# Kernel optimization log

Measured on AMD Instinct MI355X. Metric: run time of the kernel, lower is better.

## Reference

```python
import jax, jax.numpy as jnp
import numpy as np

N_NODES = 100000

def _sage_conv(x, src, dst, W_l, b_l, W_r):
    # PyG SAGEConv(aggr='mean'): out = lin_l(mean_{j in N(i)} x_j) + lin_r(x_i)
    agg = jax.ops.segment_sum(x[src], dst, num_segments=N_NODES)          # [N, F]
    cnt = jax.ops.segment_sum(jnp.ones_like(dst, dtype=x.dtype), dst,
                              num_segments=N_NODES)                        # [N]
    mean = agg / jnp.maximum(cnt, 1.0)[:, None]
    return mean @ W_l + b_l + x @ W_r

def setup_inputs() -> dict:
    key = jax.random.key(0)
    ks = jax.random.split(key, 10)
    F_in, H = 128, 16
    E, P = 1600000, 2000000
    x = jax.random.normal(ks[0], (N_NODES, F_in), dtype=jnp.float32)
    edge_index = jax.random.randint(ks[1], (2, E), 0, N_NODES, dtype=jnp.int64)
    decode_index = jax.random.randint(ks[2], (2, P), 0, N_NODES, dtype=jnp.int64)
    s1 = 1.0 / np.sqrt(F_in)
    s2 = 1.0 / np.sqrt(H)
    W1l = jax.random.uniform(ks[3], (F_in, H), jnp.float32, -s1, s1)
    b1 = jax.random.uniform(ks[4], (H,), jnp.float32, -s1, s1)
    W1r = jax.random.uniform(ks[5], (F_in, H), jnp.float32, -s1, s1)
    W2l = jax.random.uniform(ks[6], (H, H), jnp.float32, -s2, s2)
    b2 = jax.random.uniform(ks[7], (H,), jnp.float32, -s2, s2)
    W2r = jax.random.uniform(ks[8], (H, H), jnp.float32, -s2, s2)
    return {"x": x, "W1l": W1l, "b1": b1, "W1r": W1r,
            "W2l": W2l, "b2": b2, "W2r": W2r,
            "edge_index": edge_index, "decode_index": decode_index}

def reference(x, W1l, b1, W1r, W2l, b2, W2r, edge_index, decode_index):
    src, dst = edge_index[0], edge_index[1]
    h = _sage_conv(x, src, dst, W1l, b1, W1r)          # conv1
    h = jax.nn.relu(h)                                  # relu (dropout: eval -> identity)
    h = _sage_conv(h, src, dst, W2l, b2, W2r)           # conv2
    logits = jnp.sum(h[decode_index[0]] * h[decode_index[1]], axis=1)  # [P]
    return jax.nn.sigmoid(logits)
```

## Files before the change

kernel.cpp:

```cpp
#include <hip/hip_runtime.h>
#include <hip/hip_fp16.h>

#define N_NODES 100000
#define F_IN 128
#define H 16
#define NBIN 391
#define BINCAP 4608
#define ECHUNK 2048
#define LIN1B 782
#define QSCALE 4096.0f
#define QINV (1.0f / 4096.0f)

__device__ inline unsigned int packi16(float a, float b) {
  int ia = __float2int_rn(fminf(fmaxf(a * QSCALE, -32767.f), 32767.f));
  int ib = __float2int_rn(fminf(fmaxf(b * QSCALE, -32767.f), 32767.f));
  return (unsigned int)((ia & 0xffff) | (ib << 16));
}

__global__ void __launch_bounds__(512) k_init(int* __restrict__ binCur) {
  int t = threadIdx.x;
  if (t < NBIN) binCur[t] = t * BINCAP;
}

__global__ void __launch_bounds__(256) k_front(
    const float* __restrict__ x, const float* __restrict__ W1l,
    const float* __restrict__ W1r, unsigned short* __restrict__ y1l,
    float* __restrict__ y1r, const int* __restrict__ src,
    const int* __restrict__ dst, int* __restrict__ binCur,
    int* __restrict__ recs, int E) {
  __shared__ float smem[2 * H * 128];
  int t = threadIdx.x;
  if (blockIdx.x < LIN1B) {
    float* red = smem;
    int part = __builtin_amdgcn_readfirstlane(t >> 7);
    int ln = t & 127;
    int n = blockIdx.x * 128 + ln;
    int nc = (n < N_NODES) ? n : (N_NODES - 1);
    const float4* xr = (const float4*)(x + (size_t)nc * F_IN + part * (F_IN / 2));
    float4 xv[16];
#pragma unroll
    for (int j = 0; j < 16; ++j) xv[j] = xr[j];
    const float* Wl = W1l + part * (F_IN / 2) * H;
    const float* Wr = W1r + part * (F_IN / 2) * H;
    float al[H], ar[H];
#pragma unroll
    for (int c = 0; c < H; ++c) { al[c] = 0.f; ar[c] = 0.f; }
#pragma unroll
    for (int j = 0; j < 16; ++j) {
      float xs[4] = {xv[j].x, xv[j].y, xv[j].z, xv[j].w};
#pragma unroll
      for (int jj = 0; jj < 4; ++jj) {
        int k = j * 4 + jj;
#pragma unroll
        for (int c = 0; c < H; ++c) {
          al[c] = fmaf(xs[jj], Wl[k * H + c], al[c]);
          ar[c] = fmaf(xs[jj], Wr[k * H + c], ar[c]);
        }
      }
    }
    if (part == 1) {
#pragma unroll
      for (int c = 0; c < H; ++c) {
        red[c * 128 + ln] = al[c];
        red[(H + c) * 128 + ln] = ar[c];
      }
    }
    __syncthreads();
    if (part == 0 && n < N_NODES) {
#pragma unroll
      for (int c = 0; c < H; ++c) {
        al[c] += red[c * 128 + ln];
        ar[c] += red[(H + c) * 128 + ln];
      }
      uint4 w0, w1;
      w0.x = packi16(al[0], al[1]);  w0.y = packi16(al[2], al[3]);
      w0.z = packi16(al[4], al[5]);  w0.w = packi16(al[6], al[7]);
      w1.x = packi16(al[8], al[9]);  w1.y = packi16(al[10], al[11]);
      w1.z = packi16(al[12], al[13]); w1.w = packi16(al[14], al[15]);
      uint4* ol = (uint4*)(y1l + (size_t)n * H);
      ol[0] = w0;
      ol[1] = w1;
      float4* orr = (float4*)(y1r + (size_t)n * H);
#pragma unroll
      for (int q = 0; q < 4; ++q)
        orr[q] = make_float4(ar[4 * q], ar[4 * q + 1], ar[4 * q + 2], ar[4 * q + 3]);
    }
  } else {
    int* hist = (int*)smem;
    int* gbase = hist + 512;
    int* cnt2 = gbase + 512;
    hist[t] = 0; hist[256 + t] = 0;
    cnt2[t] = 0; cnt2[256 + t] = 0;
    __syncthreads();
    int base = (blockIdx.x - LIN1B) * ECHUNK;
    int rec[8], bin[8];
#pragma unroll
    for (int j = 0; j < 8; ++j) {
      int e = base + j * 256 + t;
      if (e < E) {
        int s = src[e];
        int d = dst[e];
        rec[j] = (s << 8) | (d & 255);
        bin[j] = d >> 8;
        atomicAdd(&hist[bin[j]], 1);
      } else {
        bin[j] = -1;
      }
    }
    __syncthreads();
    for (int u = t; u < NBIN; u += 256) {
      int c = hist[u];
      gbase[u] = (c > 0) ? atomicAdd(&binCur[u], c) : 0;
    }
    __syncthreads();
#pragma unroll
    for (int j = 0; j < 8; ++j) {
      if (bin[j] >= 0) {
        int loc = atomicAdd(&cnt2[bin[j]], 1);
        int slot = gbase[bin[j]] + loc;
        if (slot < (bin[j] + 1) * BINCAP)
          recs[slot] = rec[j];
      }
    }
  }
}

__global__ void __launch_bounds__(512) k_group(
    int* __restrict__ recs, const int* __restrict__ binCur,
    int* __restrict__ deg, int* __restrict__ rowBeg) {
  __shared__ int lrec[BINCAP];
  __shared__ int hist[256];
  __shared__ int off[256];
  __shared__ int cur[256];
  int t = threadIdx.x;
  int b = blockIdx.x;
  int rbase = b * BINCAP;
  int R = binCur[b] - rbase;
  if (R > BINCAP) R = BINCAP;
  if (t < 256) hist[t] = 0;
  __syncthreads();
#pragma unroll
  for (int j = 0; j < 9; ++j) {
    int idx = j * 512 + t;
    if (idx < R) {
      int r = recs[rbase + idx];
      lrec[idx] = r;
      atomicAdd(&hist[r & 255], 1);
    }
  }
  __syncthreads();
  if (t < 256) off[t] = hist[t];
  __syncthreads();
  for (int o = 1; o < 256; o <<= 1) {
    int u = 0;
    if (t < 256 && t >= o) u = off[t - o];
    __syncthreads();
    if (t < 256) off[t] += u;
    __syncthreads();
  }
  if (t < 256) {
    int ex = off[t] - hist[t];
    cur[t] = ex;
    int n = (b << 8) + t;
    if (n < N_NODES) {
      deg[n] = hist[t];
      rowBeg[n] = rbase + ex;
    }
  }
  __syncthreads();
#pragma unroll
  for (int j = 0; j < 9; ++j) {
    int idx = j * 512 + t;
    if (idx < R) {
      int r = lrec[idx];
      int slot = atomicAdd(&cur[r & 255], 1);
      recs[rbase + slot] = r >> 8;
    }
  }
}

__global__ void __launch_bounds__(256) k_gather1(
    const int* __restrict__ srcSorted, const int* __restrict__ deg,
    const int* __restrict__ rowBeg, const unsigned short* __restrict__ y1l,
    const float* __restrict__ y1r, const float* __restrict__ b1,
    const float* __restrict__ W2l, const float* __restrict__ W2r,
    unsigned short* __restrict__ z2l, float* __restrict__ z2r) {
  int tid = blockIdx.x * 256 + threadIdx.x;
  int n = tid >> 2;
  int q = tid & 3;
  if (n >= N_NODES) return;
  int beg = rowBeg[n];
  int dg = deg[n];
  int end = beg + dg;
  int acc0 = 0, acc1 = 0, acc2 = 0, acc3 = 0;
  int i = beg;
  for (; i + 8 <= end; i += 8) {
    int sqa = srcSorted[i + q];
    int sqb = srcSorted[i + 4 + q];
#pragma unroll
    for (int j = 0; j < 4; ++j) {
      int sa = __shfl(sqa, j, 4);
      int sb = __shfl(sqb, j, 4);
      uint2 va = *(const uint2*)(y1l + (size_t)sa * H + q * 4);
      uint2 vb = *(const uint2*)(y1l + (size_t)sb * H + q * 4);
      acc0 += (((int)(va.x << 16)) >> 16) + (((int)(vb.x << 16)) >> 16);
      acc1 += (((int)va.x) >> 16) + (((int)vb.x) >> 16);
      acc2 += (((int)(va.y << 16)) >> 16) + (((int)(vb.y << 16)) >> 16);
      acc3 += (((int)va.y) >> 16) + (((int)vb.y) >> 16);
    }
  }
  for (; i + 4 <= end; i += 4) {
    int sq = srcSorted[i + q];
#pragma unroll
    for (int j = 0; j < 4; ++j) {
      int sj = __shfl(sq, j, 4);
      uint2 v = *(const uint2*)(y1l + (size_t)sj * H + q * 4);
      acc0 += ((int)(v.x << 16)) >> 16;
      acc1 += ((int)v.x) >> 16;
      acc2 += ((int)(v.y << 16)) >> 16;
      acc3 += ((int)v.y) >> 16;
    }
  }
  for (; i < end; ++i) {
    int sj = srcSorted[i];
    uint2 v = *(const uint2*)(y1l + (size_t)sj * H + q * 4);
    acc0 += ((int)(v.x << 16)) >> 16;
    acc1 += ((int)v.x) >> 16;
    acc2 += ((int)(v.y << 16)) >> 16;
    acc3 += ((int)v.y) >> 16;
  }
  float s = (1.f / fmaxf((float)dg, 1.f)) * QINV;
  float4 yr = *(const float4*)(y1r + (size_t)n * H + q * 4);
  float4 bb = *(const float4*)(b1 + q * 4);
  float h1x = fmaxf(fmaf((float)acc0, s, bb.x + yr.x), 0.f);
  float h1y = fmaxf(fmaf((float)acc1, s, bb.y + yr.y), 0.f);
  float h1z = fmaxf(fmaf((float)acc2, s, bb.z + yr.z), 0.f);
  float h1w = fmaxf(fmaf((float)acc3, s, bb.w + yr.w), 0.f);
  float zl0 = 0.f, zl1 = 0.f, zl2 = 0.f, zl3 = 0.f;
  float zr0 = 0.f, zr1 = 0.f, zr2 = 0.f, zr3 = 0.f;
#pragma unroll
  for (int sl = 0; sl < 4; ++sl) {
    float hx = __shfl(h1x, sl, 4);
    float hy = __shfl(h1y, sl, 4);
    float hz = __shfl(h1z, sl, 4);
    float hw = __shfl(h1w, sl, 4);
    float hk4[4] = {hx, hy, hz, hw};
#pragma unroll
    for (int j = 0; j < 4; ++j) {
      int k = sl * 4 + j;
      float4 wl = *(const float4*)(W2l + k * H + q * 4);
      float4 wr = *(const float4*)(W2r + k * H + q * 4);
      float hk = hk4[j];
      zl0 = fmaf(hk, wl.x, zl0); zl1 = fmaf(hk, wl.y, zl1);
      zl2 = fmaf(hk, wl.z, zl2); zl3 = fmaf(hk, wl.w, zl3);
      zr0 = fmaf(hk, wr.x, zr0); zr1 = fmaf(hk, wr.y, zr1);
      zr2 = fmaf(hk, wr.z, zr2); zr3 = fmaf(hk, wr.w, zr3);
    }
  }
  uint2 pk;
  pk.x = packi16(zl0, zl1);
  pk.y = packi16(zl2, zl3);
  *(uint2*)(z2l + (size_t)n * H + q * 4) = pk;
  *(float4*)(z2r + (size_t)n * H + q * 4) = make_float4(zr0, zr1, zr2, zr3);
}

__global__ void __launch_bounds__(256) k_gather2(
    const int* __restrict__ srcSorted, const int* __restrict__ deg,
    const int* __restrict__ rowBeg, const unsigned short* __restrict__ z2l,
    const float* __restrict__ z2r, const float* __restrict__ b2,
    __half* __restrict__ h2) {
  int tid = blockIdx.x * 256 + threadIdx.x;
  int n = tid >> 2;
  int q = tid & 3;
  if (n >= N_NODES) return;
  int beg = rowBeg[n];
  int dg = deg[n];
  int end = beg + dg;
  int acc0 = 0, acc1 = 0, acc2 = 0, acc3 = 0;
  int i = beg;
  for (; i + 8 <= end; i += 8) {
    int sqa = srcSorted[i + q];
    int sqb = srcSorted[i + 4 + q];
#pragma unroll
    for (int j = 0; j < 4; ++j) {
      int sa = __shfl(sqa, j, 4);
      int sb = __shfl(sqb, j, 4);
      uint2 va = *(const uint2*)(z2l + (size_t)sa * H + q * 4);
      uint2 vb = *(const uint2*)(z2l + (size_t)sb * H + q * 4);
      acc0 += (((int)(va.x << 16)) >> 16) + (((int)(vb.x << 16)) >> 16);
      acc1 += (((int)va.x) >> 16) + (((int)vb.x) >> 16);
      acc2 += (((int)(va.y << 16)) >> 16) + (((int)(vb.y << 16)) >> 16);
      acc3 += (((int)va.y) >> 16) + (((int)vb.y) >> 16);
    }
  }
  for (; i + 4 <= end; i += 4) {
    int sq = srcSorted[i + q];
#pragma unroll
    for (int j = 0; j < 4; ++j) {
      int sj = __shfl(sq, j, 4);
      uint2 v = *(const uint2*)(z2l + (size_t)sj * H + q * 4);
      acc0 += ((int)(v.x << 16)) >> 16;
      acc1 += ((int)v.x) >> 16;
      acc2 += ((int)(v.y << 16)) >> 16;
      acc3 += ((int)v.y) >> 16;
    }
  }
  for (; i < end; ++i) {
    int sj = srcSorted[i];
    uint2 v = *(const uint2*)(z2l + (size_t)sj * H + q * 4);
    acc0 += ((int)(v.x << 16)) >> 16;
    acc1 += ((int)v.x) >> 16;
    acc2 += ((int)(v.y << 16)) >> 16;
    acc3 += ((int)v.y) >> 16;
  }
  float s = (1.f / fmaxf((float)dg, 1.f)) * QINV;
  float4 zr = *(const float4*)(z2r + (size_t)n * H + q * 4);
  float4 bb = *(const float4*)(b2 + q * 4);
  float v0 = fmaf((float)acc0, s, bb.x + zr.x);
  float v1 = fmaf((float)acc1, s, bb.y + zr.y);
  float v2 = fmaf((float)acc2, s, bb.z + zr.z);
  float v3 = fmaf((float)acc3, s, bb.w + zr.w);
  __half2 h0 = __floats2half2_rn(v0, v1);
  __half2 h1 = __floats2half2_rn(v2, v3);
  uint2 pk;
  pk.x = *(unsigned int*)&h0;
  pk.y = *(unsigned int*)&h1;
  *(uint2*)(h2 + (size_t)n * H + q * 4) = pk;
}

__device__ inline float dot8h(uint4 u, uint4 v) {
  float acc = 0.f;
  const unsigned int* uw = (const unsigned int*)&u;
  const unsigned int* vw = (const unsigned int*)&v;
#pragma unroll
  for (int j = 0; j < 4; ++j) {
    float2 a = __half22float2(*(const __half2*)&uw[j]);
    float2 b = __half22float2(*(const __half2*)&vw[j]);
    acc = fmaf(a.x, b.x, acc);
    acc = fmaf(a.y, b.y, acc);
  }
  return acc;
}

__global__ void __launch_bounds__(256) k_decode(
    const int* __restrict__ ps, const int* __restrict__ pd,
    const __half* __restrict__ h2, float* __restrict__ out, int P) {
  int t = blockIdx.x * 256 + threadIdx.x;
  int p = t * 2;
  if (p >= P) return;
  int2 av = *(const int2*)(ps + p);
  int2 bv = *(const int2*)(pd + p);
  const uint4* ha0 = (const uint4*)(h2 + (size_t)av.x * H);
  const uint4* hb0 = (const uint4*)(h2 + (size_t)bv.x * H);
  const uint4* ha1 = (const uint4*)(h2 + (size_t)av.y * H);
  const uint4* hb1 = (const uint4*)(h2 + (size_t)bv.y * H);
  uint4 u00 = ha0[0], u01 = ha0[1];
  uint4 v00 = hb0[0], v01 = hb0[1];
  uint4 u10 = ha1[0], u11 = ha1[1];
  uint4 v10 = hb1[0], v11 = hb1[1];
  float d0 = dot8h(u00, v00) + dot8h(u01, v01);
  float d1 = dot8h(u10, v10) + dot8h(u11, v11);
  float o0 = 1.f / (1.f + __expf(-d0));
  float o1 = 1.f / (1.f + __expf(-d1));
  if (p + 1 < P) {
    *(float2*)(out + p) = make_float2(o0, o1);
  } else {
    out[p] = o0;
  }
}

extern "C" void kernel_launch(void* const* d_in, const int* in_sizes, int n_in,
                              void* d_out, int out_size, void* d_ws, size_t ws_size,
                              hipStream_t stream) {
  const float* x   = (const float*)d_in[0];
  const float* W1l = (const float*)d_in[1];
  const float* b1  = (const float*)d_in[2];
  const float* W1r = (const float*)d_in[3];
  const float* W2l = (const float*)d_in[4];
  const float* b2  = (const float*)d_in[5];
  const float* W2r = (const float*)d_in[6];
  const int* ei = (const int*)d_in[7];
  const int* di = (const int*)d_in[8];
  const int E = in_sizes[7] / 2;
  const int P = in_sizes[8] / 2;

  const size_t NF = (size_t)N_NODES * H;
  unsigned short* y1l = (unsigned short*)d_ws;
  __half*         h2  = (__half*)y1l;
  unsigned short* z2l = y1l + NF;
  float*  y1r = (float*)(z2l + NF);
  float*  z2r = y1r;
  int* recs   = (int*)(y1r + NF);
  int* binCur = recs + (size_t)NBIN * BINCAP;
  int* deg    = binCur + 512;
  int* rowBeg = deg + N_NODES;

  const int fillBlocks = (E + ECHUNK - 1) / ECHUNK;
  const int frontBlocks = LIN1B + fillBlocks;
  const int gatherBlocks = ((N_NODES * 4) + 255) / 256;
  const int decodeBlocks = ((P + 1) / 2 + 255) / 256;

  k_init<<<1, 512, 0, stream>>>(binCur);
  k_front<<<frontBlocks, 256, 0, stream>>>(x, W1l, W1r, y1l, y1r,
                                           ei, ei + E, binCur, recs, E);
  k_group<<<NBIN, 512, 0, stream>>>(recs, binCur, deg, rowBeg);
  k_gather1<<<gatherBlocks, 256, 0, stream>>>(recs, deg, rowBeg, y1l, y1r,
                                              b1, W2l, W2r, z2l, z2r);
  k_gather2<<<gatherBlocks, 256, 0, stream>>>(recs, deg, rowBeg, z2l, z2r,
                                              b2, h2);
  k_decode<<<decodeBlocks, 256, 0, stream>>>(di, di + P, h2, (float*)d_out, P);
}
```

Measured before the change: 225.5 us.

## Split fused front kernel into separate lin1 and edge bin-fill kernels

Splits the combined kernel, which ran the dense first-layer projection and the edge binning in one launch, into two launches. The projection now handles 64 nodes per block with the 128 input features split four ways across threads instead of two, and combines the partial sums through shared memory. The binning kernel now processes 8192 edges per 512-thread block, which cuts the number of global atomics on the bin cursors. The split gives up the overlap between the compute-bound and atomic-bound work that the fused launch allowed, and adds one extra launch.

After: 213.6 us. 1.06x faster.

```diff
diff --git a/kernel.cpp b/kernel.cpp
--- a/kernel.cpp
+++ b/kernel.cpp
@@ -6,8 +6,7 @@
 #define H 16
 #define NBIN 391
 #define BINCAP 4608
-#define ECHUNK 2048
-#define LIN1B 782
+#define ECHUNK 8192
 #define QSCALE 4096.0f
 #define QINV (1.0f / 4096.0f)
 
@@ -22,105 +21,108 @@
   if (t < NBIN) binCur[t] = t * BINCAP;
 }
 
-__global__ void __launch_bounds__(256) k_front(
+__global__ void __launch_bounds__(256) k_lin1(
     const float* __restrict__ x, const float* __restrict__ W1l,
     const float* __restrict__ W1r, unsigned short* __restrict__ y1l,
-    float* __restrict__ y1r, const int* __restrict__ src,
-    const int* __restrict__ dst, int* __restrict__ binCur,
-    int* __restrict__ recs, int E) {
-  __shared__ float smem[2 * H * 128];
+    float* __restrict__ y1r) {
+  __shared__ float red[3 * 32 * 64];
   int t = threadIdx.x;
-  if (blockIdx.x < LIN1B) {
-    float* red = smem;
-    int part = __builtin_amdgcn_readfirstlane(t >> 7);
-    int ln = t & 127;
-    int n = blockIdx.x * 128 + ln;
-    int nc = (n < N_NODES) ? n : (N_NODES - 1);
-    const float4* xr = (const float4*)(x + (size_t)nc * F_IN + part * (F_IN / 2));
-    float4 xv[16];
-#pragma unroll
-    for (int j = 0; j < 16; ++j) xv[j] = xr[j];
-    const float* Wl = W1l + part * (F_IN / 2) * H;
-    const float* Wr = W1r + part * (F_IN / 2) * H;
-    float al[H], ar[H];
-#pragma unroll
-    for (int c = 0; c < H; ++c) { al[c] = 0.f; ar[c] = 0.f; }
-#pragma unroll
-    for (int j = 0; j < 16; ++j) {
-      float xs[4] = {xv[j].x, xv[j].y, xv[j].z, xv[j].w};
-#pragma unroll
-      for (int jj = 0; jj < 4; ++jj) {
-        int k = j * 4 + jj;
-#pragma unroll
-        for (int c = 0; c < H; ++c) {
-          al[c] = fmaf(xs[jj], Wl[k * H + c], al[c]);
-          ar[c] = fmaf(xs[jj], Wr[k * H + c], ar[c]);
-        }
+  int part = __builtin_amdgcn_readfirstlane(t >> 6);
+  int ln = t & 63;
+  int n = blockIdx.x * 64 + ln;
+  int nc = (n < N_NODES) ? n : (N_NODES - 1);
+  const float4* xr = (const float4*)(x + (size_t)nc * F_IN + part * (F_IN / 4));
+  float4 xv[8];
+#pragma unroll
+  for (int j = 0; j < 8; ++j) xv[j] = xr[j];
+  const float* Wl = W1l + part * (F_IN / 4) * H;
+  const float* Wr = W1r + part * (F_IN / 4) * H;
+  float al[H], ar[H];
+#pragma unroll
+  for (int c = 0; c < H; ++c) { al[c] = 0.f; ar[c] = 0.f; }
+#pragma unroll
+  for (int j = 0; j < 8; ++j) {
+    float xs[4] = {xv[j].x, xv[j].y, xv[j].z, xv[j].w};
+#pragma unroll
+    for (int jj = 0; jj < 4; ++jj) {
+      int k = j * 4 + jj;
+#pragma unroll
+      for (int c = 0; c < H; ++c) {
+        al[c] = fmaf(xs[jj], Wl[k * H + c], al[c]);
+        ar[c] = fmaf(xs[jj], Wr[k * H + c], ar[c]);
       }
     }
-    if (part == 1) {
-#pragma unroll
-      for (int c = 0; c < H; ++c) {
-        red[c * 128 + ln] = al[c];
-        red[(H + c) * 128 + ln] = ar[c];
-      }
-    }
-    __syncthreads();
-    if (part == 0 && n < N_NODES) {
-#pragma unroll
-      for (int c = 0; c < H; ++c) {
-        al[c] += red[c * 128 + ln];
-        ar[c] += red[(H + c) * 128 + ln];
-      }
-      uint4 w0, w1;
-      w0.x = packi16(al[0], al[1]);  w0.y = packi16(al[2], al[3]);
-      w0.z = packi16(al[4], al[5]);  w0.w = packi16(al[6], al[7]);
-      w1.x = packi16(al[8], al[9]);  w1.y = packi16(al[10], al[11]);
-      w1.z = packi16(al[12], al[13]); w1.w = packi16(al[14], al[15]);
-      uint4* ol = (uint4*)(y1l + (size_t)n * H);
-      ol[0] = w0;
-      ol[1] = w1;
-      float4* orr = (float4*)(y1r + (size_t)n * H);
-#pragma unroll
-      for (int q = 0; q < 4; ++q)
-        orr[q] = make_float4(ar[4 * q], ar[4 * q + 1], ar[4 * q + 2], ar[4 * q + 3]);
-    }
-  } else {
-    int* hist = (int*)smem;
-    int* gbase = hist + 512;
-    int* cnt2 = gbase + 512;
-    hist[t] = 0; hist[256 + t] = 0;
-    cnt2[t] = 0; cnt2[256 + t] = 0;
-    __syncthreads();
-    int base = (blockIdx.x - LIN1B) * ECHUNK;
-    int rec[8], bin[8];
-#pragma unroll
-    for (int j = 0; j < 8; ++j) {
-      int e = base + j * 256 + t;
-      if (e < E) {
-        int s = src[e];
-        int d = dst[e];
-        rec[j] = (s << 8) | (d & 255);
-        bin[j] = d >> 8;
-        atomicAdd(&hist[bin[j]], 1);
-      } else {
-        bin[j] = -1;
-      }
-    }
-    __syncthreads();
-    for (int u = t; u < NBIN; u += 256) {
-      int c = hist[u];
-      gbase[u] = (c > 0) ? atomicAdd(&binCur[u], c) : 0;
-    }
-    __syncthreads();
-#pragma unroll
-    for (int j = 0; j < 8; ++j) {
-      if (bin[j] >= 0) {
-        int loc = atomicAdd(&cnt2[bin[j]], 1);
-        int slot = gbase[bin[j]] + loc;
-        if (slot < (bin[j] + 1) * BINCAP)
-          recs[slot] = rec[j];
-      }
+  }
+  if (part != 0) {
+    int base = (part - 1) * 2048;
+#pragma unroll
+    for (int c = 0; c < H; ++c) {
+      red[base + c * 64 + ln] = al[c];
+      red[base + (H + c) * 64 + ln] = ar[c];
+    }
+  }
+  __syncthreads();
+  if (part == 0 && n < N_NODES) {
+#pragma unroll
+    for (int c = 0; c < H; ++c) {
+      al[c] = ((al[c] + red[c * 64 + ln]) + red[2048 + c * 64 + ln])
+              + red[4096 + c * 64 + ln];
+      ar[c] = ((ar[c] + red[(H + c) * 64 + ln]) + red[2048 + (H + c) * 64 + ln])
+              + red[4096 + (H + c) * 64 + ln];
+    }
+    uint4 w0, w1;
+    w0.x = packi16(al[0], al[1]);  w0.y = packi16(al[2], al[3]);
+    w0.z = packi16(al[4], al[5]);  w0.w = packi16(al[6], al[7]);
+    w1.x = packi16(al[8], al[9]);  w1.y = packi16(al[10], al[11]);
+    w1.z = packi16(al[12], al[13]); w1.w = packi16(al[14], al[15]);
+    uint4* ol = (uint4*)(y1l + (size_t)n * H);
+    ol[0] = w0;
+    ol[1] = w1;
+    float4* orr = (float4*)(y1r + (size_t)n * H);
+#pragma unroll
+    for (int q = 0; q < 4; ++q)
+      orr[q] = make_float4(ar[4 * q], ar[4 * q + 1], ar[4 * q + 2], ar[4 * q + 3]);
+  }
+}
+
+__global__ void __launch_bounds__(512) k_binfill(
+    const int* __restrict__ src, const int* __restrict__ dst,
+    int* __restrict__ binCur, int* __restrict__ recs, int E) {
+  __shared__ int hist[512];
+  __shared__ int gbase[512];
+  __shared__ int cnt2[512];
+  int t = threadIdx.x;
+  hist[t] = 0;
+  cnt2[t] = 0;
+  __syncthreads();
+  int base = blockIdx.x * ECHUNK;
+  int rec[16], bin[16];
+#pragma unroll
+  for (int j = 0; j < 16; ++j) {
+    int e = base + j * 512 + t;
+    if (e < E) {
+      int s = src[e];
+      int d = dst[e];
+      rec[j] = (s << 8) | (d & 255);
+      bin[j] = d >> 8;
+      atomicAdd(&hist[bin[j]], 1);
+    } else {
+      bin[j] = -1;
+    }
+  }
+  __syncthreads();
+  if (t < NBIN) {
+    int c = hist[t];
+    gbase[t] = (c > 0) ? atomicAdd(&binCur[t], c) : 0;
+  }
+  __syncthreads();
+#pragma unroll
+  for (int j = 0; j < 16; ++j) {
+    if (bin[j] >= 0) {
+      int loc = atomicAdd(&cnt2[bin[j]], 1);
+      int slot = gbase[bin[j]] + loc;
+      if (slot < (bin[j] + 1) * BINCAP)
+        recs[slot] = rec[j];
     }
   }
 }
@@ -395,14 +397,14 @@
   int* deg    = binCur + 512;
   int* rowBeg = deg + N_NODES;
 
+  const int lin1Blocks = (N_NODES + 63) / 64;
   const int fillBlocks = (E + ECHUNK - 1) / ECHUNK;
-  const int frontBlocks = LIN1B + fillBlocks;
   const int gatherBlocks = ((N_NODES * 4) + 255) / 256;
   const int decodeBlocks = ((P + 1) / 2 + 255) / 256;
 
   k_init<<<1, 512, 0, stream>>>(binCur);
-  k_front<<<frontBlocks, 256, 0, stream>>>(x, W1l, W1r, y1l, y1r,
-                                           ei, ei + E, binCur, recs, E);
+  k_lin1<<<lin1Blocks, 256, 0, stream>>>(x, W1l, W1r, y1l, y1r);
+  k_binfill<<<fillBlocks, 512, 0, stream>>>(ei, ei + E, binCur, recs, E);
   k_group<<<NBIN, 512, 0, stream>>>(recs, binCur, deg, rowBeg);
   k_gather1<<<gatherBlocks, 256, 0, stream>>>(recs, deg, rowBeg, y1l, y1r,
                                               b1, W2l, W2r, z2l, z2r);
```
